# Optimization experiments

Hardware: AMD Instinct MI355X
Metric: run time of the kernel (lower is better)

## Reference

```python
import jax, jax.numpy as jnp
import numpy as np

B, S, E, H, NQ, FF = 2, 2048, 768, 12, 8, 3072
DK = E // H
EPS = 1e-5


def _layernorm(x, g, b):
    m = jnp.mean(x, axis=-1, keepdims=True)
    v = jnp.mean((x - m) ** 2, axis=-1, keepdims=True)
    return (x - m) * jax.lax.rsqrt(v + EPS) * g + b


def setup_inputs() -> dict:
    key = jax.random.key(0)
    ks = jax.random.split(key, 12)
    s = 0.02
    return {
        'x': jax.random.normal(ks[0], (B, S, E), dtype=jnp.float32),
        'W_o': jax.random.normal(ks[1], (E, E), dtype=jnp.float32) * s,
        'b_o': jnp.zeros((E,), dtype=jnp.float32),
        'g1': jnp.ones((E,), dtype=jnp.float32),
        'be1': jnp.zeros((E,), dtype=jnp.float32),
        'g2': jnp.ones((E,), dtype=jnp.float32),
        'be2': jnp.zeros((E,), dtype=jnp.float32),
        'ry': jax.random.normal(ks[2], (NQ,), dtype=jnp.float32),
        'W1': jax.random.normal(ks[3], (NQ, FF), dtype=jnp.float32) * s,
        'b1': jnp.zeros((FF,), dtype=jnp.float32),
        'W2': jax.random.normal(ks[4], (FF, E), dtype=jnp.float32) * s,
        'b2': jnp.zeros((E,), dtype=jnp.float32),
    }


def reference(x, W_o, b_o, g1, be1, g2, be2, ry, W1, b1, W2, b2):
    # --- multi-head self-attention (q = k = v = x, no QKV projection) ---
    q = x.reshape(B, S, H, DK).transpose(0, 2, 1, 3)  # [B,H,S,DK]
    scores = jnp.einsum('bhqd,bhkd->bhqk', q, q) / jnp.sqrt(jnp.float32(DK))
    attn = jax.nn.softmax(scores, axis=-1)
    out = jnp.einsum('bhqk,bhkd->bhqd', attn, q)
    out = out.transpose(0, 2, 1, 3).reshape(B, S, E)
    attn_out = out @ W_o + b_o

    x = _layernorm(x + attn_out, g1, be1)

    # --- quantum FFN: per-wire RX(x_i) encode, RY(ry_i), <Z> = cos(x_i)*cos(ry_i) ---
    q_meas = jnp.cos(x[..., :NQ]) * jnp.cos(ry)  # [B,S,NQ]
    ffn_out = jax.nn.relu(q_meas @ W1 + b1) @ W2 + b2

    return _layernorm(x + ffn_out, g2, be2)
```

## Files before the change

### kernel.cpp

```cpp
#include <hip/hip_runtime.h>
#include <hip/hip_bf16.h>

#define B_  2
#define S_  2048
#define E_  768
#define H_  12
#define DK_ 64
#define NQ_ 8
#define FF_ 3072
#define EPS_ 1e-5f

typedef __attribute__((ext_vector_type(8))) short short8;
typedef __attribute__((ext_vector_type(4))) float f32x4;
typedef __hip_bfloat16 bf16;

__device__ __forceinline__ bf16 f2bh(float f) { return __float2bfloat16(f); }
__device__ __forceinline__ short f2b(float f) {
    bf16 h = __float2bfloat16(f);
    return *reinterpret_cast<short*>(&h);
}

__device__ __forceinline__ int swz(int row, int col) {
    return (col & 7) | ((((col >> 3) ^ (row & 7)) & 7) << 3);
}

__device__ __forceinline__ f32x4 mfma16(short8 a, short8 b, f32x4 c) {
    return __builtin_amdgcn_mfma_f32_16x16x32_bf16(a, b, c, 0, 0, 0);
}

__global__ __launch_bounds__(256) void prep_xall(const float* __restrict__ x,
                                                 bf16* __restrict__ xb,
                                                 bf16* __restrict__ xT) {
    __shared__ float tile[32][33];
    int e0 = blockIdx.x * 32, s0 = blockIdx.y * 32;
    int tx = threadIdx.x & 31, ty = threadIdx.x >> 5;
    int b = s0 >> 11, sl0 = s0 & 2047;
#pragma unroll
    for (int i = 0; i < 4; i++) {
        int row = ty + i * 8;
        float v = x[(size_t)(s0 + row) * E_ + e0 + tx];
        tile[row][tx] = v;
        xb[(size_t)(s0 + row) * E_ + e0 + tx] = f2bh(v);
    }
    __syncthreads();
#pragma unroll
    for (int i = 0; i < 4; i++) {
        int row = ty + i * 8;
        xT[((size_t)b * E_ + e0 + row) * S_ + sl0 + tx] = f2bh(tile[tx][row]);
    }
}

__global__ __launch_bounds__(256) void prep_cvt(const float* __restrict__ x,
                                                bf16* __restrict__ xb, int n4) {
    int i = blockIdx.x * 256 + threadIdx.x;
    if (i >= n4) return;
    float4 f = *(const float4*)(x + (size_t)i * 4);
    short4 sv;
    sv.x = f2b(f.x); sv.y = f2b(f.y); sv.z = f2b(f.z); sv.w = f2b(f.w);
    *(short4*)((short*)xb + (size_t)i * 4) = sv;
}

__global__ __launch_bounds__(256) void transpose_cvt(const float* __restrict__ W,
                                                     bf16* __restrict__ WT,
                                                     int K, int N) {
    __shared__ float tile[32][33];
    int k0 = blockIdx.y * 32, n0 = blockIdx.x * 32;
    int tx = threadIdx.x & 31, ty = threadIdx.x >> 5;
#pragma unroll
    for (int i = 0; i < 4; i++) {
        int row = ty + i * 8;
        tile[row][tx] = W[(size_t)(k0 + row) * N + n0 + tx];
    }
    __syncthreads();
#pragma unroll
    for (int i = 0; i < 4; i++) {
        int row = ty + i * 8;
        WT[(size_t)(n0 + row) * K + k0 + tx] = f2bh(tile[tx][row]);
    }
}

__global__ __launch_bounds__(256) void prep_w1t(const float* __restrict__ W1,
                                                bf16* __restrict__ W1bT) {
    int k = blockIdx.x * 256 + threadIdx.x;
    if (k >= FF_) return;
    short8 v;
#pragma unroll
    for (int i = 0; i < NQ_; i++) v[i] = f2b(W1[(size_t)i * FF_ + k]);
    *(short8*)(W1bT + (size_t)k * NQ_) = v;
}

template<bool XT>
__global__ __launch_bounds__(256) void attn_kernel(const bf16* __restrict__ xb,
                                                   const bf16* __restrict__ xT,
                                                   bf16* __restrict__ out) {
    const int qtiles = S_ / 64;
    const int nwg = B_ * H_ * qtiles;
    int o = blockIdx.x;
    int blk = (o & 7) * (nwg >> 3) + (o >> 3);
    int qt = blk % qtiles;
    int hh = (blk / qtiles) % H_;
    int bb = blk / (qtiles * H_);
    const bf16* base = xb + (size_t)bb * S_ * E_ + hh * DK_;
    const bf16* baseT = xT + ((size_t)bb * E_ + hh * DK_) * S_;

    __shared__ __align__(16) bf16 Ks[64][64];
    __shared__ __align__(16) bf16 Vt[64][64];
    __shared__ __align__(16) bf16 Pl[4][16][64];

    int t = threadIdx.x;
    int w = t >> 6, l = t & 63, c = l & 15, g = l >> 4;

    short8 qf[2];
    {
        const bf16* qp = base + (size_t)(qt * 64 + w * 16 + c) * E_;
        qf[0] = *(const short8*)(qp + g * 8);
        qf[1] = *(const short8*)(qp + 32 + g * 8);
    }

    f32x4 oacc[4];
    float l_part[4];
#pragma unroll
    for (int n = 0; n < 4; n++) { oacc[n] = (f32x4){0.f, 0.f, 0.f, 0.f}; l_part[n] = 0.f; }

    int skey = t & 63;
    int scb0 = t >> 6;

    short8 preK[2], preV[2];
#pragma unroll
    for (int it = 0; it < 2; it++) {
        preK[it] = *(const short8*)(base + (size_t)skey * E_ + (scb0 + it * 4) * 8);
        if (XT)
            preV[it] = *(const short8*)(baseT + (size_t)skey * S_ + (scb0 + it * 4) * 8);
    }

    for (int kt = 0; kt < S_ / 64; kt++) {
#pragma unroll
        for (int it = 0; it < 2; it++) {
            int cb = scb0 + it * 4;
            *(short8*)&Ks[skey][swz(skey, cb * 8)] = preK[it];
            if (XT) {
                *(short8*)&Vt[skey][swz(skey, cb * 8)] = preV[it];
            } else {
#pragma unroll
                for (int j = 0; j < 8; j++) {
                    int d = cb * 8 + j;
                    short sv = preK[it][j];
                    Vt[d][swz(d, skey)] = *reinterpret_cast<bf16*>(&sv);
                }
            }
        }
        __syncthreads();

        if (kt + 1 < S_ / 64) {
#pragma unroll
            for (int it = 0; it < 2; it++) {
                preK[it] = *(const short8*)(base + (size_t)((kt + 1) * 64 + skey) * E_ + (scb0 + it * 4) * 8);
                if (XT)
                    preV[it] = *(const short8*)(baseT + (size_t)skey * S_ + (kt + 1) * 64 + (scb0 + it * 4) * 8);
            }
        }

        f32x4 sfr[4];
        __builtin_amdgcn_s_setprio(1);
#pragma unroll
        for (int n = 0; n < 4; n++) {
            sfr[n] = (f32x4){0.f, 0.f, 0.f, 0.f};
#pragma unroll
            for (int kh = 0; kh < 2; kh++) {
                const short8 bfr = *(const short8*)&Ks[n * 16 + c][swz(n * 16 + c, kh * 32 + g * 8)];
                sfr[n] = mfma16(qf[kh], bfr, sfr[n]);
            }
        }
        __builtin_amdgcn_s_setprio(0);
#pragma unroll
        for (int jj = 0; jj < 4; jj++) {
            float pv[4];
#pragma unroll
            for (int n = 0; n < 4; n++)
                pv[n] = exp2f(sfr[n][jj] * 0.18033688f);
            l_part[jj] += (pv[0] + pv[1]) + (pv[2] + pv[3]);
            int r = g * 4 + jj;
#pragma unroll
            for (int n = 0; n < 4; n++)
                Pl[w][r][swz(r, n * 16 + c)] = f2bh(pv[n]);
        }

        __builtin_amdgcn_s_setprio(1);
#pragma unroll
        for (int ks = 0; ks < 2; ks++) {
            short8 vb[4];
#pragma unroll
            for (int dn = 0; dn < 4; dn++)
                vb[dn] = *(const short8*)&Vt[dn * 16 + c][swz(dn * 16 + c, ks * 32 + g * 8)];
            const short8 pa = *(const short8*)&Pl[w][c][swz(c, ks * 32 + g * 8)];
#pragma unroll
            for (int dn = 0; dn < 4; dn++)
                oacc[dn] = mfma16(pa, vb[dn], oacc[dn]);
        }
        __builtin_amdgcn_s_setprio(0);
        __syncthreads();
    }

#pragma unroll
    for (int jj = 0; jj < 4; jj++) {
        float lv = l_part[jj];
#pragma unroll
        for (int msk = 1; msk < 16; msk <<= 1) lv += __shfl_xor(lv, msk);
        float inv = 1.f / lv;
        size_t ro = ((size_t)bb * S_ + qt * 64 + w * 16 + g * 4 + jj) * E_ + hh * DK_;
#pragma unroll
        for (int dn = 0; dn < 4; dn++)
            out[ro + dn * 16 + c] = f2bh(oacc[dn][jj] * inv);
    }
}

__global__ __launch_bounds__(256) void gemm_bf16(const bf16* __restrict__ A,
                                                 const bf16* __restrict__ BT,
                                                 const float* __restrict__ bias,
                                                 bf16* __restrict__ C,
                                                 int M, int N, int K) {
    __shared__ __align__(16) bf16 As2[2][64][64];
    __shared__ __align__(16) bf16 Bs2[2][64][64];
    int nbx = gridDim.x, nwg = nbx * gridDim.y;
    int id = blockIdx.y * nbx + blockIdx.x;
    int id2 = (nwg & 7) ? id : ((id & 7) * (nwg >> 3) + (id >> 3));
    int row0 = (id2 / nbx) * 64, col0 = (id2 % nbx) * 64;
    int t = threadIdx.x, w = t >> 6, l = t & 63, c = l & 15, g = l >> 4;

    f32x4 acc[4];
#pragma unroll
    for (int n = 0; n < 4; n++) acc[n] = (f32x4){0.f, 0.f, 0.f, 0.f};

    int srow = t & 63, scb = t >> 6;
    const bf16* ap = A + (size_t)(row0 + srow) * K;
    const bf16* bp = BT + (size_t)(col0 + srow) * K;

    short8 pA0, pA1, pB0, pB1;
    pA0 = *(const short8*)(ap + scb * 8);
    pA1 = *(const short8*)(ap + (scb + 4) * 8);
    pB0 = *(const short8*)(bp + scb * 8);
    pB1 = *(const short8*)(bp + (scb + 4) * 8);
    *(short8*)&As2[0][srow][swz(srow, scb * 8)] = pA0;
    *(short8*)&As2[0][srow][swz(srow, (scb + 4) * 8)] = pA1;
    *(short8*)&Bs2[0][srow][swz(srow, scb * 8)] = pB0;
    *(short8*)&Bs2[0][srow][swz(srow, (scb + 4) * 8)] = pB1;
    if (64 < K) {
        pA0 = *(const short8*)(ap + 64 + scb * 8);
        pA1 = *(const short8*)(ap + 64 + (scb + 4) * 8);
        pB0 = *(const short8*)(bp + 64 + scb * 8);
        pB1 = *(const short8*)(bp + 64 + (scb + 4) * 8);
    }
    __syncthreads();

    int cur = 0;
    for (int k0 = 0; k0 < K; k0 += 64, cur ^= 1) {
        int nxt = cur ^ 1;
        if (k0 + 64 < K) {
            *(short8*)&As2[nxt][srow][swz(srow, scb * 8)] = pA0;
            *(short8*)&As2[nxt][srow][swz(srow, (scb + 4) * 8)] = pA1;
            *(short8*)&Bs2[nxt][srow][swz(srow, scb * 8)] = pB0;
            *(short8*)&Bs2[nxt][srow][swz(srow, (scb + 4) * 8)] = pB1;
        }
        if (k0 + 128 < K) {
            pA0 = *(const short8*)(ap + k0 + 128 + scb * 8);
            pA1 = *(const short8*)(ap + k0 + 128 + (scb + 4) * 8);
            pB0 = *(const short8*)(bp + k0 + 128 + scb * 8);
            pB1 = *(const short8*)(bp + k0 + 128 + (scb + 4) * 8);
        }
#pragma unroll
        for (int kh = 0; kh < 2; kh++) {
            const short8 af = *(const short8*)&As2[cur][w * 16 + c][swz(w * 16 + c, kh * 32 + g * 8)];
#pragma unroll
            for (int n = 0; n < 4; n++) {
                const short8 bfr = *(const short8*)&Bs2[cur][n * 16 + c][swz(n * 16 + c, kh * 32 + g * 8)];
                acc[n] = mfma16(af, bfr, acc[n]);
            }
        }
        __syncthreads();
    }
#pragma unroll
    for (int jj = 0; jj < 4; jj++) {
        int row = row0 + w * 16 + g * 4 + jj;
#pragma unroll
        for (int n = 0; n < 4; n++) {
            int col = col0 + n * 16 + c;
            C[(size_t)row * N + col] = f2bh(acc[n][jj] + bias[col]);
        }
    }
}

__global__ __launch_bounds__(256) void gemm2_mfma(const float* __restrict__ xln,
                                                  const float* __restrict__ ry,
                                                  const bf16* __restrict__ W1bT,
                                                  const float* __restrict__ b1,
                                                  const bf16* __restrict__ W2bT,
                                                  const float* __restrict__ b2,
                                                  bf16* __restrict__ C) {
    __shared__ __align__(16) bf16 As[64][64];
    __shared__ __align__(16) bf16 Bs[2][64][64];
    __shared__ __align__(16) bf16 W1t[2][64][8];
    __shared__ __align__(16) bf16 qm_s[64][8];
    const int nbx = E_ / 64;
    const int nwg = nbx * (B_ * S_ / 64);
    int id = blockIdx.y * nbx + blockIdx.x;
    int id2 = (id & 7) * (nwg >> 3) + (id >> 3);
    int row0 = (id2 / nbx) * 64, col0 = (id2 % nbx) * 64;
    int t = threadIdx.x, w = t >> 6, l = t & 63, c = l & 15, g = l >> 4;

    if (t < 64) {
        const float* xp = xln + (size_t)(row0 + t) * E_;
#pragma unroll
        for (int i = 0; i < NQ_; i++)
            qm_s[t][i] = f2bh(cosf(xp[i]) * cosf(ry[i]));
    }

    f32x4 acc[4];
#pragma unroll
    for (int n = 0; n < 4; n++) acc[n] = (f32x4){0.f, 0.f, 0.f, 0.f};

    int srow = t & 63, scb = t >> 6;
    const bf16* brow_p = W2bT + (size_t)(col0 + srow) * FF_;

    short8 preB0, preB1, preW;
    preB0 = *(const short8*)(brow_p + scb * 8);
    preB1 = *(const short8*)(brow_p + (scb + 4) * 8);
    if (t < 64) preW = *(const short8*)(W1bT + (size_t)t * NQ_);
    *(short8*)&Bs[0][srow][swz(srow, scb * 8)] = preB0;
    *(short8*)&Bs[0][srow][swz(srow, (scb + 4) * 8)] = preB1;
    if (t < 64) *(short8*)&W1t[0][t][0] = preW;
    preB0 = *(const short8*)(brow_p + 64 + scb * 8);
    preB1 = *(const short8*)(brow_p + 64 + (scb + 4) * 8);
    if (t < 64) preW = *(const short8*)(W1bT + (size_t)(64 + t) * NQ_);
    __syncthreads();

    short8 zz = {0, 0, 0, 0, 0, 0, 0, 0};
    short8 aq = zz;
    if (g == 0) aq = *(const short8*)&qm_s[w * 16 + c][0];

    int cur = 0;
    for (int k0 = 0; k0 < FF_; k0 += 64, cur ^= 1) {
        float b1c[4];
#pragma unroll
        for (int n = 0; n < 4; n++) b1c[n] = b1[k0 + n * 16 + c];

        int nxt = cur ^ 1;
        if (k0 + 64 < FF_) {
            *(short8*)&Bs[nxt][srow][swz(srow, scb * 8)] = preB0;
            *(short8*)&Bs[nxt][srow][swz(srow, (scb + 4) * 8)] = preB1;
            if (t < 64) *(short8*)&W1t[nxt][t][0] = preW;
        }
        if (k0 + 128 < FF_) {
            preB0 = *(const short8*)(brow_p + k0 + 128 + scb * 8);
            preB1 = *(const short8*)(brow_p + k0 + 128 + (scb + 4) * 8);
            if (t < 64) preW = *(const short8*)(W1bT + (size_t)(k0 + 128 + t) * NQ_);
        }

        f32x4 zero4 = {0.f, 0.f, 0.f, 0.f};
#pragma unroll
        for (int n = 0; n < 4; n++) {
            short8 bw = zz;
            if (g == 0) bw = *(const short8*)&W1t[cur][n * 16 + c][0];
            f32x4 hfr = mfma16(aq, bw, zero4);
#pragma unroll
            for (int jj = 0; jj < 4; jj++) {
                float hv = fmaxf(hfr[jj] + b1c[n], 0.f);
                int r = w * 16 + g * 4 + jj;
                As[r][swz(r, n * 16 + c)] = f2bh(hv);
            }
        }

#pragma unroll
        for (int kh = 0; kh < 2; kh++) {
            const short8 af = *(const short8*)&As[w * 16 + c][swz(w * 16 + c, kh * 32 + g * 8)];
#pragma unroll
            for (int n = 0; n < 4; n++) {
                const short8 bfr = *(const short8*)&Bs[cur][n * 16 + c][swz(n * 16 + c, kh * 32 + g * 8)];
                acc[n] = mfma16(af, bfr, acc[n]);
            }
        }
        __syncthreads();
    }
#pragma unroll
    for (int jj = 0; jj < 4; jj++) {
        int row = row0 + w * 16 + g * 4 + jj;
#pragma unroll
        for (int n = 0; n < 4; n++) {
            int col = col0 + n * 16 + c;
            C[(size_t)row * E_ + col] = f2bh(acc[n][jj] + b2[col]);
        }
    }
}

__global__ __launch_bounds__(256) void gemm2_fused(const float* __restrict__ xln,
                                                   const float* __restrict__ ry,
                                                   const float* __restrict__ W1,
                                                   const float* __restrict__ b1,
                                                   const float* __restrict__ W2,
                                                   const float* __restrict__ b2,
                                                   bf16* __restrict__ C) {
    __shared__ __align__(16) bf16 As[64][64];
    __shared__ __align__(16) bf16 Bst[64][64];
    __shared__ float qmS[64][NQ_];
    int row0 = blockIdx.y * 64, col0 = blockIdx.x * 64;
    int t = threadIdx.x, w = t >> 6, l = t & 63, c = l & 15, g = l >> 4;

    for (int idx = t; idx < 64 * NQ_; idx += 256) {
        int r = idx >> 3, i = idx & 7;
        qmS[r][i] = cosf(xln[(size_t)(row0 + r) * E_ + i]) * cosf(ry[i]);
    }

    f32x4 acc[4];
#pragma unroll
    for (int n = 0; n < 4; n++) acc[n] = (f32x4){0.f, 0.f, 0.f, 0.f};

    int kl = t & 63, rg = (t >> 6) * 16;
    int brow = t >> 4, bcol = (t & 15) * 4;

    for (int k0 = 0; k0 < FF_; k0 += 64) {
        __syncthreads();
        {
            float w1v[NQ_];
#pragma unroll
            for (int i = 0; i < NQ_; i++) w1v[i] = W1[i * FF_ + k0 + kl];
            float b1v = b1[k0 + kl];
#pragma unroll
            for (int r16 = 0; r16 < 16; r16++) {
                int r = rg + r16;
                float sh = b1v;
#pragma unroll
                for (int i = 0; i < NQ_; i++) sh += qmS[r][i] * w1v[i];
                As[r][swz(r, kl)] = f2bh(fmaxf(sh, 0.f));
            }
        }
#pragma unroll
        for (int it = 0; it < 4; it++) {
            int kk = brow + it * 16;
            float4 v = *(const float4*)(W2 + (size_t)(k0 + kk) * E_ + col0 + bcol);
            Bst[bcol + 0][swz(bcol + 0, kk)] = f2bh(v.x);
            Bst[bcol + 1][swz(bcol + 1, kk)] = f2bh(v.y);
            Bst[bcol + 2][swz(bcol + 2, kk)] = f2bh(v.z);
            Bst[bcol + 3][swz(bcol + 3, kk)] = f2bh(v.w);
        }
        __syncthreads();
#pragma unroll
        for (int kh = 0; kh < 2; kh++) {
            const short8 af = *(const short8*)&As[w * 16 + c][swz(w * 16 + c, kh * 32 + g * 8)];
#pragma unroll
            for (int n = 0; n < 4; n++) {
                const short8 bfr = *(const short8*)&Bst[n * 16 + c][swz(n * 16 + c, kh * 32 + g * 8)];
                acc[n] = mfma16(af, bfr, acc[n]);
            }
        }
    }
#pragma unroll
    for (int jj = 0; jj < 4; jj++) {
        int row = row0 + w * 16 + g * 4 + jj;
#pragma unroll
        for (int n = 0; n < 4; n++) {
            int col = col0 + n * 16 + c;
            C[(size_t)row * E_ + col] = f2bh(acc[n][jj] + b2[col]);
        }
    }
}

__global__ __launch_bounds__(256) void ln_add_b(const float* __restrict__ X,
                                                const bf16* __restrict__ Yb,
                                                const float* __restrict__ g,
                                                const float* __restrict__ be,
                                                float* __restrict__ out) {
    int r = blockIdx.x;
    const size_t off = (size_t)r * E_;
    int t = threadIdx.x;
    float v[3];
    float s = 0.f, s2 = 0.f;
#pragma unroll
    for (int j = 0; j < 3; j++) {
        int e = t + j * 256;
        float val = X[off + e] + __bfloat162float(Yb[off + e]);
        v[j] = val; s += val; s2 += val * val;
    }
#pragma unroll
    for (int msk = 32; msk > 0; msk >>= 1) {
        s += __shfl_xor(s, msk);
        s2 += __shfl_xor(s2, msk);
    }
    __shared__ float red[8];
    int lane = t & 63, wv = t >> 6;
    if (lane == 0) { red[wv] = s; red[4 + wv] = s2; }
    __syncthreads();
    if (t == 0) {
        red[0] = red[0] + red[1] + red[2] + red[3];
        red[4] = red[4] + red[5] + red[6] + red[7];
    }
    __syncthreads();
    float mean = red[0] * (1.f / E_);
    float var = red[4] * (1.f / E_) - mean * mean;
    float inv = rsqrtf(var + EPS_);
#pragma unroll
    for (int j = 0; j < 3; j++) {
        int e = t + j * 256;
        out[off + e] = (v[j] - mean) * inv * g[e] + be[e];
    }
}

extern "C" void kernel_launch(void* const* d_in, const int* in_sizes, int n_in,
                              void* d_out, int out_size, void* d_ws, size_t ws_size,
                              hipStream_t stream) {
    const float* x   = (const float*)d_in[0];
    const float* W_o = (const float*)d_in[1];
    const float* b_o = (const float*)d_in[2];
    const float* g1  = (const float*)d_in[3];
    const float* be1 = (const float*)d_in[4];
    const float* g2  = (const float*)d_in[5];
    const float* be2 = (const float*)d_in[6];
    const float* ry  = (const float*)d_in[7];
    const float* W1  = (const float*)d_in[8];
    const float* b1  = (const float*)d_in[9];
    const float* W2  = (const float*)d_in[10];
    const float* b2  = (const float*)d_in[11];
    float* out = (float*)d_out;

    const size_t BSE = (size_t)B_ * S_ * E_;
    char* ws = (char*)d_ws;

    const size_t FAST_NEED = 43696128;
    bool fast = ws_size >= FAST_NEED;

    bf16* xb    = (bf16*)(ws + 0);
    bf16* attnb = (bf16*)(ws + 6291456);
    bf16* WobT  = fast ? (bf16*)(ws + 12582912) : (bf16*)(ws + 18874368);
    bf16* W2bT  = (bf16*)(ws + 13762560);
    bf16* tmp1b = fast ? (bf16*)(ws + 18481152) : (bf16*)(ws + 12582912);
    float* xln  = (float*)(ws + (fast ? 24772608 : 20054016));
    bf16* W1bT  = (bf16*)(ws + 37355520);
    bf16* xT    = (bf16*)(ws + 37404672);
    bf16* tmp2b = tmp1b;

    if (fast) {
        prep_xall<<<dim3(E_ / 32, B_ * S_ / 32), 256, 0, stream>>>(x, xb, xT);
        transpose_cvt<<<dim3(E_ / 32, FF_ / 32), 256, 0, stream>>>(W2, W2bT, FF_, E_);
        prep_w1t<<<dim3(FF_ / 256), 256, 0, stream>>>(W1, W1bT);
    } else {
        prep_cvt<<<dim3((int)((BSE / 4 + 255) / 256)), 256, 0, stream>>>(x, xb, (int)(BSE / 4));
    }
    transpose_cvt<<<dim3(E_ / 32, E_ / 32), 256, 0, stream>>>(W_o, WobT, E_, E_);

    if (fast)
        attn_kernel<true><<<dim3(B_ * H_ * (S_ / 64)), 256, 0, stream>>>(xb, xT, attnb);
    else
        attn_kernel<false><<<dim3(B_ * H_ * (S_ / 64)), 256, 0, stream>>>(xb, xb, attnb);

    gemm_bf16<<<dim3(E_ / 64, (B_ * S_) / 64), 256, 0, stream>>>(
        attnb, WobT, b_o, tmp1b, B_ * S_, E_, E_);
    ln_add_b<<<dim3(B_ * S_), 256, 0, stream>>>(x, tmp1b, g1, be1, xln);

    if (fast) {
        gemm2_mfma<<<dim3(E_ / 64, (B_ * S_) / 64), 256, 0, stream>>>(
            xln, ry, W1bT, b1, W2bT, b2, tmp2b);
    } else {
        gemm2_fused<<<dim3(E_ / 64, (B_ * S_) / 64), 256, 0, stream>>>(
            xln, ry, W1, b1, W2, b2, tmp2b);
    }
    ln_add_b<<<dim3(B_ * S_), 256, 0, stream>>>(xln, tmp2b, g2, be2, out);
}
```

Before: 174.6 us.

## Software-pipeline the hidden-activation tile one step ahead in fused FFN GEMM

The fused FFN kernel now computes the ReLU(q·W1+b1) hidden tile for the next K-step while the current step's W2 MFMAs run, using a double-buffered As tile. W1 and b1 slices are loaded straight from global memory into registers one step early, instead of being staged through shared memory. The aim is to take the dependent first-layer MFMA and its LDS write off the critical path before the main MFMAs in each iteration. In exchange it uses more registers and more LDS for the second As buffer, which could lower occupancy.

```diff
diff --git a/kernel.cpp b/kernel.cpp
--- a/kernel.cpp
+++ b/kernel.cpp
@@ -296,12 +296,12 @@
                                                   const bf16* __restrict__ W2bT,
                                                   const float* __restrict__ b2,
                                                   bf16* __restrict__ C) {
-    __shared__ __align__(16) bf16 As[64][64];
+    __shared__ __align__(16) bf16 As[2][64][64];
     __shared__ __align__(16) bf16 Bs[2][64][64];
-    __shared__ __align__(16) bf16 W1t[2][64][8];
     __shared__ __align__(16) bf16 qm_s[64][8];
     const int nbx = E_ / 64;
     const int nwg = nbx * (B_ * S_ / 64);
+    const int NS = FF_ / 64;
     int id = blockIdx.y * nbx + blockIdx.x;
     int id2 = (id & 7) * (nwg >> 3) + (id >> 3);
     int row0 = (id2 / nbx) * 64, col0 = (id2 % nbx) * 64;
@@ -321,61 +321,86 @@
     int srow = t & 63, scb = t >> 6;
     const bf16* brow_p = W2bT + (size_t)(col0 + srow) * FF_;
 
-    short8 preB0, preB1, preW;
+    const short8 zz = {0, 0, 0, 0, 0, 0, 0, 0};
+    const f32x4 zero4 = {0.f, 0.f, 0.f, 0.f};
+
+    short8 preB0, preB1;
     preB0 = *(const short8*)(brow_p + scb * 8);
     preB1 = *(const short8*)(brow_p + (scb + 4) * 8);
-    if (t < 64) preW = *(const short8*)(W1bT + (size_t)t * NQ_);
     *(short8*)&Bs[0][srow][swz(srow, scb * 8)] = preB0;
     *(short8*)&Bs[0][srow][swz(srow, (scb + 4) * 8)] = preB1;
-    if (t < 64) *(short8*)&W1t[0][t][0] = preW;
     preB0 = *(const short8*)(brow_p + 64 + scb * 8);
     preB1 = *(const short8*)(brow_p + 64 + (scb + 4) * 8);
-    if (t < 64) preW = *(const short8*)(W1bT + (size_t)(64 + t) * NQ_);
     __syncthreads();
 
-    short8 zz = {0, 0, 0, 0, 0, 0, 0, 0};
     short8 aq = zz;
     if (g == 0) aq = *(const short8*)&qm_s[w * 16 + c][0];
 
+    short8 bwN[4];
+    float b1N[4];
+#pragma unroll
+    for (int n = 0; n < 4; n++) {
+        bwN[n] = zz;
+        if (g == 0) bwN[n] = *(const short8*)(W1bT + (size_t)(n * 16 + c) * NQ_);
+        b1N[n] = b1[n * 16 + c];
+    }
+#pragma unroll
+    for (int n = 0; n < 4; n++) {
+        f32x4 hfr = mfma16(aq, bwN[n], zero4);
+#pragma unroll
+        for (int jj = 0; jj < 4; jj++) {
+            int r = w * 16 + g * 4 + jj;
+            As[0][r][swz(r, n * 16 + c)] = f2bh(fmaxf(hfr[jj] + b1N[n], 0.f));
+        }
+    }
+#pragma unroll
+    for (int n = 0; n < 4; n++) {
+        bwN[n] = zz;
+        if (g == 0) bwN[n] = *(const short8*)(W1bT + (size_t)(64 + n * 16 + c) * NQ_);
+        b1N[n] = b1[64 + n * 16 + c];
+    }
+
     int cur = 0;
     for (int k0 = 0; k0 < FF_; k0 += 64, cur ^= 1) {
-        float b1c[4];
-#pragma unroll
-        for (int n = 0; n < 4; n++) b1c[n] = b1[k0 + n * 16 + c];
-
         int nxt = cur ^ 1;
         if (k0 + 64 < FF_) {
             *(short8*)&Bs[nxt][srow][swz(srow, scb * 8)] = preB0;
             *(short8*)&Bs[nxt][srow][swz(srow, (scb + 4) * 8)] = preB1;
-            if (t < 64) *(short8*)&W1t[nxt][t][0] = preW;
         }
         if (k0 + 128 < FF_) {
             preB0 = *(const short8*)(brow_p + k0 + 128 + scb * 8);
             preB1 = *(const short8*)(brow_p + k0 + 128 + (scb + 4) * 8);
-            if (t < 64) preW = *(const short8*)(W1bT + (size_t)(k0 + 128 + t) * NQ_);
-        }
-
-        f32x4 zero4 = {0.f, 0.f, 0.f, 0.f};
-#pragma unroll
-        for (int n = 0; n < 4; n++) {
-            short8 bw = zz;
-            if (g == 0) bw = *(const short8*)&W1t[cur][n * 16 + c][0];
-            f32x4 hfr = mfma16(aq, bw, zero4);
-#pragma unroll
-            for (int jj = 0; jj < 4; jj++) {
-                float hv = fmaxf(hfr[jj] + b1c[n], 0.f);
-                int r = w * 16 + g * 4 + jj;
-                As[r][swz(r, n * 16 + c)] = f2bh(hv);
-            }
-        }
-
+        }
+        f32x4 hfr[4];
+        if (k0 + 64 < FF_) {
+#pragma unroll
+            for (int n = 0; n < 4; n++) hfr[n] = mfma16(aq, bwN[n], zero4);
+        }
 #pragma unroll
         for (int kh = 0; kh < 2; kh++) {
-            const short8 af = *(const short8*)&As[w * 16 + c][swz(w * 16 + c, kh * 32 + g * 8)];
+            const short8 af = *(const short8*)&As[cur][w * 16 + c][swz(w * 16 + c, kh * 32 + g * 8)];
 #pragma unroll
             for (int n = 0; n < 4; n++) {
                 const short8 bfr = *(const short8*)&Bs[cur][n * 16 + c][swz(n * 16 + c, kh * 32 + g * 8)];
                 acc[n] = mfma16(af, bfr, acc[n]);
+            }
+        }
+        if (k0 + 64 < FF_) {
+#pragma unroll
+            for (int n = 0; n < 4; n++) {
+#pragma unroll
+                for (int jj = 0; jj < 4; jj++) {
+                    int r = w * 16 + g * 4 + jj;
+                    As[nxt][r][swz(r, n * 16 + c)] = f2bh(fmaxf(hfr[n][jj] + b1N[n], 0.f));
+                }
+            }
+        }
+        if (k0 + 128 < FF_) {
+#pragma unroll
+            for (int n = 0; n < 4; n++) {
+                bwN[n] = zz;
+                if (g == 0) bwN[n] = *(const short8*)(W1bT + (size_t)(k0 + 128 + n * 16 + c) * NQ_);
+                b1N[n] = b1[k0 + 128 + n * 16 + c];
             }
         }
         __syncthreads();
```

Result: slower. 186.2 us (+6.6%).

## Double-buffer K/V shared-memory tiles in attention kernel to drop a barrier

Applied to the files above, without the earlier changes.

Ks and Vt in shared memory become two-slot ping-pong buffers. Each iteration stores the prefetched next tile into the spare slot while computing on the current one, and registers are prefetched two tiles ahead. This removes one of the two __syncthreads per key tile and lets the shared-memory stores overlap the MFMA work. In exchange, LDS use per workgroup roughly doubles for K/V, which may reduce how many workgroups fit on a CU.

```diff
diff --git a/kernel.cpp b/kernel.cpp
--- a/kernel.cpp
+++ b/kernel.cpp
@@ -103,8 +103,8 @@
     const bf16* base = xb + (size_t)bb * S_ * E_ + hh * DK_;
     const bf16* baseT = xT + ((size_t)bb * E_ + hh * DK_) * S_;
 
-    __shared__ __align__(16) bf16 Ks[64][64];
-    __shared__ __align__(16) bf16 Vt[64][64];
+    __shared__ __align__(16) bf16 Ks[2][64][64];
+    __shared__ __align__(16) bf16 Vt[2][64][64];
     __shared__ __align__(16) bf16 Pl[4][16][64];
 
     int t = threadIdx.x;
@@ -132,31 +132,55 @@
         if (XT)
             preV[it] = *(const short8*)(baseT + (size_t)skey * S_ + (scb0 + it * 4) * 8);
     }
-
-    for (int kt = 0; kt < S_ / 64; kt++) {
-#pragma unroll
-        for (int it = 0; it < 2; it++) {
-            int cb = scb0 + it * 4;
-            *(short8*)&Ks[skey][swz(skey, cb * 8)] = preK[it];
-            if (XT) {
-                *(short8*)&Vt[skey][swz(skey, cb * 8)] = preV[it];
-            } else {
-#pragma unroll
-                for (int j = 0; j < 8; j++) {
-                    int d = cb * 8 + j;
-                    short sv = preK[it][j];
-                    Vt[d][swz(d, skey)] = *reinterpret_cast<bf16*>(&sv);
+#pragma unroll
+    for (int it = 0; it < 2; it++) {
+        int cb = scb0 + it * 4;
+        *(short8*)&Ks[0][skey][swz(skey, cb * 8)] = preK[it];
+        if (XT) {
+            *(short8*)&Vt[0][skey][swz(skey, cb * 8)] = preV[it];
+        } else {
+#pragma unroll
+            for (int j = 0; j < 8; j++) {
+                int d = cb * 8 + j;
+                short sv = preK[it][j];
+                Vt[0][d][swz(d, skey)] = *reinterpret_cast<bf16*>(&sv);
+            }
+        }
+    }
+#pragma unroll
+    for (int it = 0; it < 2; it++) {
+        preK[it] = *(const short8*)(base + (size_t)(64 + skey) * E_ + (scb0 + it * 4) * 8);
+        if (XT)
+            preV[it] = *(const short8*)(baseT + (size_t)skey * S_ + 64 + (scb0 + it * 4) * 8);
+    }
+    __syncthreads();
+
+    int cur = 0;
+    for (int kt = 0; kt < S_ / 64; kt++, cur ^= 1) {
+        int nxt = cur ^ 1;
+        if (kt + 1 < S_ / 64) {
+#pragma unroll
+            for (int it = 0; it < 2; it++) {
+                int cb = scb0 + it * 4;
+                *(short8*)&Ks[nxt][skey][swz(skey, cb * 8)] = preK[it];
+                if (XT) {
+                    *(short8*)&Vt[nxt][skey][swz(skey, cb * 8)] = preV[it];
+                } else {
+#pragma unroll
+                    for (int j = 0; j < 8; j++) {
+                        int d = cb * 8 + j;
+                        short sv = preK[it][j];
+                        Vt[nxt][d][swz(d, skey)] = *reinterpret_cast<bf16*>(&sv);
+                    }
                 }
             }
         }
-        __syncthreads();
-
-        if (kt + 1 < S_ / 64) {
+        if (kt + 2 < S_ / 64) {
 #pragma unroll
             for (int it = 0; it < 2; it++) {
-                preK[it] = *(const short8*)(base + (size_t)((kt + 1) * 64 + skey) * E_ + (scb0 + it * 4) * 8);
+                preK[it] = *(const short8*)(base + (size_t)((kt + 2) * 64 + skey) * E_ + (scb0 + it * 4) * 8);
                 if (XT)
-                    preV[it] = *(const short8*)(baseT + (size_t)skey * S_ + (kt + 1) * 64 + (scb0 + it * 4) * 8);
+                    preV[it] = *(const short8*)(baseT + (size_t)skey * S_ + (kt + 2) * 64 + (scb0 + it * 4) * 8);
             }
         }
 
@@ -167,7 +191,7 @@
             sfr[n] = (f32x4){0.f, 0.f, 0.f, 0.f};
 #pragma unroll
             for (int kh = 0; kh < 2; kh++) {
-                const short8 bfr = *(const short8*)&Ks[n * 16 + c][swz(n * 16 + c, kh * 32 + g * 8)];
+                const short8 bfr = *(const short8*)&Ks[cur][n * 16 + c][swz(n * 16 + c, kh * 32 + g * 8)];
                 sfr[n] = mfma16(qf[kh], bfr, sfr[n]);
             }
         }
@@ -191,7 +215,7 @@
             short8 vb[4];
 #pragma unroll
             for (int dn = 0; dn < 4; dn++)
-                vb[dn] = *(const short8*)&Vt[dn * 16 + c][swz(dn * 16 + c, ks * 32 + g * 8)];
+                vb[dn] = *(const short8*)&Vt[cur][dn * 16 + c][swz(dn * 16 + c, ks * 32 + g * 8)];
             const short8 pa = *(const short8*)&Pl[w][c][swz(c, ks * 32 + g * 8)];
 #pragma unroll
             for (int dn = 0; dn < 4; dn++)
```

New measurement: 176.2 us. About the same (+0.9%).
